# Kernel tuning notes

Hardware: AMD Instinct MI355X
Metric: run time of the kernel (lower is better)

## Reference

```python
import jax, jax.numpy as jnp
import numpy as np

N, D, E, TOP_K = 4096, 1024, 8, 2
NEG_INF = -1e38


def setup_inputs() -> dict:
    key = jax.random.key(0)
    ks = jax.random.split(key, 6)
    s = 1.0 / np.sqrt(D)
    return {
        "x": jax.random.normal(ks[0], (N, D), jnp.float32),
        "noise": jax.random.normal(ks[1], (E,), jnp.float32),
        "Wg": jax.random.normal(ks[2], (D, E), jnp.float32) * s,
        "Wn": jax.random.normal(ks[3], (D, E), jnp.float32) * s,
        "We": jax.random.normal(ks[4], (E, D, D), jnp.float32) * s,
        "be": jax.random.normal(ks[5], (E, D), jnp.float32) * 0.01,
    }


def reference(x, noise, Wg, Wn, We, be):
    # Gating: H = Wg(x) + randn(E) * softplus(Wnoise(x))   (Eq. 4-5)
    g = x @ Wg                                      # [N, E]
    H = g + noise[None, :] * jax.nn.softplus(x @ Wn)  # [N, E]
    # Keep top_k entries of H, set the rest to -Inf (scatter of bottom E-k)
    vals, idx = jax.lax.top_k(H, TOP_K)             # [N, k]
    keep = jnp.full_like(H, NEG_INF)
    keep = keep.at[jnp.arange(H.shape[0])[:, None], idx].set(vals)
    G = jax.nn.softmax(keep, axis=1)                # [N, E]; masked entries -> 0
    # Expert outputs; masked experts have G==0 so dense weighted sum matches
    # the sparse per-example loop: out_n = sum_j G[n,j] * expert_j(x_n)
    Y = jnp.einsum('nd,edh->neh', x, We) + be[None, :, :]  # [N, E, D]
    out = jnp.einsum('ne,neh->nh', G, Y)            # [N, D]
    return out
```

## Files before the change

### kernel.cpp

```cpp
#include <hip/hip_runtime.h>
#include <hip/hip_bf16.h>
#include <stdint.h>

#define NR   4096
#define DIM  1024
#define NE   8
#define BM   128
#define BN   128
#define BK   32

typedef __attribute__((ext_vector_type(8))) short  bf16x8;
typedef __attribute__((ext_vector_type(8))) ushort u16x8;
typedef __attribute__((ext_vector_type(4))) float  f32x4;

__device__ __forceinline__ ushort f2bf(float f) {
    union { __hip_bfloat16 h; ushort u; } cv;
    cv.h = __float2bfloat16(f);
    return cv.u;
}

__device__ __forceinline__ void gload16(const void* g, void* l) {
    __builtin_amdgcn_global_load_lds(
        (const __attribute__((address_space(1))) unsigned int*)g,
        (__attribute__((address_space(3))) unsigned int*)l, 16, 0, 0);
}

__global__ __launch_bounds__(256)
void k1_prep(const float* __restrict__ Wg, const float* __restrict__ Wn,
             float* __restrict__ WT, float* __restrict__ out) {
    const int tid = threadIdx.x;
    if (blockIdx.x < 8) {
        const int k    = blockIdx.x * 128 + (tid >> 1);
        const int half = tid & 1;
        const float* src = half ? Wn : Wg;
        const float4* s4 = (const float4*)(src + (size_t)k * NE);
        float4 a = s4[0], b = s4[1];
        float* d = WT + (size_t)half * 8 * DIM;
        d[(size_t)0 * DIM + k] = a.x; d[(size_t)1 * DIM + k] = a.y;
        d[(size_t)2 * DIM + k] = a.z; d[(size_t)3 * DIM + k] = a.w;
        d[(size_t)4 * DIM + k] = b.x; d[(size_t)5 * DIM + k] = b.y;
        d[(size_t)6 * DIM + k] = b.z; d[(size_t)7 * DIM + k] = b.w;
    } else {
        const int vb = blockIdx.x - 8;
        float4 z = {0.f, 0.f, 0.f, 0.f};
        for (int i = vb * 256 + tid; i < NR * DIM / 4; i += 512 * 256)
            ((float4*)out)[i] = z;
    }
}

__global__ __launch_bounds__(256)
void k2_main(const float* __restrict__ We, ushort* __restrict__ WeT,
             const float* __restrict__ x, const float* __restrict__ noise,
             const float* __restrict__ WT, ushort* __restrict__ xbf,
             uint32_t* __restrict__ eid, float2* __restrict__ wpair) {
    __shared__ float smem[64 * 68];
    const int tid = threadIdx.x;
    if (blockIdx.x < 2048) {
        const int b  = blockIdx.x;
        const int e  = b >> 8, kt = (b >> 4) & 15, ct = b & 15;
        const float* src = We + ((size_t)e * DIM + (size_t)kt * 64) * DIM + ct * 64;
#pragma unroll
        for (int j = 0; j < 4; ++j) {
            int idx = tid + j * 256;
            int r = idx >> 4, c4 = idx & 15;
            *(float4*)&smem[r * 68 + c4 * 4] = *(const float4*)(src + (size_t)r * DIM + c4 * 4);
        }
        __syncthreads();
        ushort* dst = WeT + ((size_t)e * DIM + (size_t)ct * 64) * DIM + kt * 64;
#pragma unroll
        for (int j = 0; j < 2; ++j) {
            int u = tid + j * 256;
            int c = u >> 3, ch = u & 7;
            ushort tmp[8];
#pragma unroll
            for (int q = 0; q < 8; ++q) tmp[q] = f2bf(smem[(ch * 8 + q) * 68 + c]);
            *(u16x8*)(dst + (size_t)c * DIM + ch * 8) = *(u16x8*)tmp;
        }
    } else {
        const int w = tid >> 6, l = tid & 63;
        const int row = (blockIdx.x - 2048) * 4 + w;
        const float* xr = x + (size_t)row * DIM;

        float4 xv[4];
#pragma unroll
        for (int q = 0; q < 4; ++q) xv[q] = *(const float4*)(xr + q * 256 + l * 4);
#pragma unroll
        for (int q = 0; q < 4; ++q) {
            ushort4 xb;
            xb.x = f2bf(xv[q].x); xb.y = f2bf(xv[q].y);
            xb.z = f2bf(xv[q].z); xb.w = f2bf(xv[q].w);
            *(ushort4*)(xbf + (size_t)row * DIM + q * 256 + l * 4) = xb;
        }

        float acc[16];
#pragma unroll
        for (int u = 0; u < 16; ++u) {
            const float* wr_ = WT + (size_t)u * DIM + l * 4;
            float s = 0.f;
#pragma unroll
            for (int q = 0; q < 4; ++q) {
                float4 wv = *(const float4*)(wr_ + q * 256);
                s += xv[q].x * wv.x + xv[q].y * wv.y + xv[q].z * wv.z + xv[q].w * wv.w;
            }
            acc[u] = s;
        }
#pragma unroll
        for (int u = 0; u < 16; ++u) smem[(w * 64 + l) * 17 + u] = acc[u];
        asm volatile("s_waitcnt lgkmcnt(0)" ::: "memory");
        const int c = l >> 4, u = l & 15;
        float v = 0.f;
#pragma unroll
        for (int i = 0; i < 16; ++i) v += smem[(w * 64 + c * 16 + i) * 17 + u];
        v += __shfl_xor(v, 16, 64);
        v += __shfl_xor(v, 32, 64);

        const int e = l & 7;
        float ag = __shfl(v, e, 64);
        float an = __shfl(v, e + 8, 64);
        float sp = (an > 0.f) ? (an + log1pf(expf(-an))) : log1pf(expf(an));
        float H  = ag + noise[e] * sp;

        float Hh[8];
#pragma unroll
        for (int k = 0; k < 8; ++k) Hh[k] = __shfl(H, k, 64);
        if (l == 0) {
            int e0 = 0; float v0 = Hh[0];
#pragma unroll
            for (int k = 1; k < 8; ++k) if (Hh[k] > v0) { v0 = Hh[k]; e0 = k; }
            int e1 = -1; float v1 = 0.f;
#pragma unroll
            for (int k = 0; k < 8; ++k)
                if (k != e0 && (e1 < 0 || Hh[k] > v1)) { v1 = Hh[k]; e1 = k; }
            float rr = expf(v1 - v0);
            float w0 = 1.f / (1.f + rr), w1 = 1.f - w0;
            eid[row] = (uint32_t)e0 | ((uint32_t)e1 << 8);
            float2 wp; wp.x = w0; wp.y = w1;
            wpair[row] = wp;
        }
    }
}

__global__ __launch_bounds__(1024)
void bucket_build(const uint32_t* __restrict__ eid, const float2* __restrict__ wpair,
                  int* __restrict__ cnt, int* __restrict__ idxl, float* __restrict__ wl) {
    const int ex = blockIdx.x;
    __shared__ int base;
    __shared__ int wsum[16];
    if (threadIdx.x == 0) base = 0;
    const int wid = threadIdx.x >> 6, lane = threadIdx.x & 63;
    int* bidx = idxl + (size_t)ex * NR;
    float* bwl = wl + (size_t)ex * NR;

    for (int c0 = 0; c0 < NR; c0 += 1024) {
        const int row = c0 + threadIdx.x;
        const uint32_t em = eid[row];
        const bool m0 = (int)(em & 255u) == ex;
        const bool m1 = (int)((em >> 8) & 255u) == ex;
        const bool m = m0 || m1;
        const unsigned long long bal = __ballot(m);
        if (lane == 0) wsum[wid] = __popcll(bal);
        __syncthreads();
        int wbase = base;
        for (int i = 0; i < wid; ++i) wbase += wsum[i];
        const int pos = wbase + __popcll(bal & ((1ull << lane) - 1ull));
        if (m) {
            bidx[pos] = row;
            float2 wp = wpair[row];
            bwl[pos]  = m0 ? wp.x : wp.y;
        }
        __syncthreads();
        if (threadIdx.x == 0) {
            int s = 0;
#pragma unroll
            for (int i = 0; i < 16; ++i) s += wsum[i];
            base += s;
        }
        __syncthreads();
    }
    if (threadIdx.x == 0) cnt[ex] = base;
}

__global__ __launch_bounds__(256, 2)
void moe_gemm(const ushort* __restrict__ xbf, const ushort* __restrict__ WeT,
              const float* __restrict__ be, const int* __restrict__ cnt,
              const int* __restrict__ idxl, const float* __restrict__ wl,
              float* __restrict__ out) {
    __shared__ ushort lds[4][256][BK];

    const int q8 = gridDim.x >> 3;
    const int W  = (blockIdx.x & 7) * q8 + (blockIdx.x >> 3);
    const int item = W >> 3, cT = W & 7;

    int bucket = -1, tile = 0, accp = 0;
#pragma unroll
    for (int b = 0; b < NE; ++b) {
        int t = (cnt[b] + BM - 1) >> 7;
        if (bucket < 0 && item < accp + t) { bucket = b; tile = item - accp; }
        accp += t;
    }
    if (bucket < 0) return;
    const int count  = cnt[bucket];
    const int nrowsv = min(BM, count - tile * BM);
    const int e  = bucket;
    const int c0 = cT * BN;
    const int*   rows = idxl + (size_t)bucket * NR + tile * BM;
    const float* wrow = wl   + (size_t)bucket * NR + tile * BM;

    const int tid = threadIdx.x, wid = tid >> 6, lane = tid & 63;
    const int l16 = lane & 15, lhi = lane >> 4;
    const int wr = (wid >> 1) * 64, wc = (wid & 1) * 64;

    const int fs   = ((lane >> 2) ^ (lane >> 4)) & 3;
    const int csrc = ((lane & 3) ^ fs) * 8;
    const ushort* aptr[2];
    const ushort* bptr[2];
#pragma unroll
    for (int g = 0; g < 2; ++g) {
        int r = g * 64 + wid * 16 + (lane >> 2);
        aptr[g] = xbf + (size_t)rows[min(r, nrowsv - 1)] * DIM + csrc;
        int c = c0 + g * 64 + wid * 16 + (lane >> 2);
        bptr[g] = WeT + ((size_t)(e * DIM + c)) * DIM + csrc;
    }

    f32x4 acc[4][4];
#pragma unroll
    for (int m = 0; m < 4; ++m)
#pragma unroll
        for (int n = 0; n < 4; ++n) { f32x4 z = {0.f, 0.f, 0.f, 0.f}; acc[m][n] = z; }

#define STAGE_A(T, BUFI) do {                                         \
    const int _k = (T) * BK;                                          \
    _Pragma("unroll")                                                 \
    for (int g = 0; g < 2; ++g)                                       \
        gload16(aptr[g] + _k, &lds[(BUFI)][g * 64 + wid * 16][0]);    \
} while (0)
#define STAGE_B(T, BUFI) do {                                         \
    const int _k = (T) * BK;                                          \
    _Pragma("unroll")                                                 \
    for (int g = 0; g < 2; ++g)                                       \
        gload16(bptr[g] + _k, &lds[(BUFI)][128 + g * 64 + wid * 16][0]); \
} while (0)

    const int fr    = (l16 ^ (l16 >> 2)) & 3;
    const int rslot = (lhi ^ fr) * 8;

    const int NT = DIM / BK;
    STAGE_A(0, 0); STAGE_B(0, 0);
    STAGE_A(1, 1); STAGE_B(1, 1);
    STAGE_A(2, 2); STAGE_B(2, 2);
    asm volatile("s_waitcnt vmcnt(8)" ::: "memory");
    __builtin_amdgcn_s_barrier();

    for (int t = 0; t < NT; ++t) {
        const int c = t & 3;
        const ushort* base = &lds[c][0][0];
        bf16x8 af0 = *(const bf16x8*)(base + (wr + 0 * 16 + l16) * BK + rslot);
        bf16x8 af1 = *(const bf16x8*)(base + (wr + 1 * 16 + l16) * BK + rslot);
        bf16x8 bfr[4];
#pragma unroll
        for (int n = 0; n < 4; ++n)
            bfr[n] = *(const bf16x8*)(base + (128 + wc + n * 16 + l16) * BK + rslot);
        if (t + 3 < NT) STAGE_A(t + 3, (t + 3) & 3);
        __builtin_amdgcn_s_barrier();
        asm volatile("s_waitcnt lgkmcnt(0)" ::: "memory");
        __builtin_amdgcn_s_setprio(1);
#pragma unroll
        for (int n = 0; n < 4; ++n)
            acc[0][n] = __builtin_amdgcn_mfma_f32_16x16x32_bf16(af0, bfr[n], acc[0][n], 0, 0, 0);
#pragma unroll
        for (int n = 0; n < 4; ++n)
            acc[1][n] = __builtin_amdgcn_mfma_f32_16x16x32_bf16(af1, bfr[n], acc[1][n], 0, 0, 0);
        __builtin_amdgcn_s_setprio(0);
        __builtin_amdgcn_s_barrier();
        bf16x8 af2 = *(const bf16x8*)(base + (wr + 2 * 16 + l16) * BK + rslot);
        bf16x8 af3 = *(const bf16x8*)(base + (wr + 3 * 16 + l16) * BK + rslot);
        if (t + 3 < NT) STAGE_B(t + 3, (t + 3) & 3);
        __builtin_amdgcn_s_barrier();
        asm volatile("s_waitcnt lgkmcnt(0)" ::: "memory");
        __builtin_amdgcn_s_setprio(1);
#pragma unroll
        for (int n = 0; n < 4; ++n)
            acc[2][n] = __builtin_amdgcn_mfma_f32_16x16x32_bf16(af2, bfr[n], acc[2][n], 0, 0, 0);
#pragma unroll
        for (int n = 0; n < 4; ++n)
            acc[3][n] = __builtin_amdgcn_mfma_f32_16x16x32_bf16(af3, bfr[n], acc[3][n], 0, 0, 0);
        __builtin_amdgcn_s_setprio(0);
        if (t < NT - 3)       asm volatile("s_waitcnt vmcnt(8)" ::: "memory");
        else if (t == NT - 3) asm volatile("s_waitcnt vmcnt(4)" ::: "memory");
        else                  asm volatile("s_waitcnt vmcnt(0)" ::: "memory");
        __builtin_amdgcn_s_barrier();
    }
#undef STAGE_A
#undef STAGE_B

    float bev[4];
#pragma unroll
    for (int n = 0; n < 4; ++n) bev[n] = be[(size_t)e * DIM + c0 + wc + n * 16 + l16];
#pragma unroll
    for (int m = 0; m < 4; ++m) {
#pragma unroll
        for (int r = 0; r < 4; ++r) {
            int rl = wr + m * 16 + lhi * 4 + r;
            if (rl < nrowsv) {
                int   gr = rows[rl];
                float w  = wrow[rl];
                float* op = out + (size_t)gr * DIM + c0 + wc;
#pragma unroll
                for (int n = 0; n < 4; ++n)
                    atomicAdd(&op[n * 16 + l16], w * (acc[m][n][r] + bev[n]));
            }
        }
    }
}

extern "C" void kernel_launch(void* const* d_in, const int* in_sizes, int n_in,
                              void* d_out, int out_size, void* d_ws, size_t ws_size,
                              hipStream_t stream) {
    const float* x     = (const float*)d_in[0];
    const float* noise = (const float*)d_in[1];
    const float* Wg    = (const float*)d_in[2];
    const float* Wn    = (const float*)d_in[3];
    const float* We    = (const float*)d_in[4];
    const float* be    = (const float*)d_in[5];
    float* out = (float*)d_out;

    char* w = (char*)d_ws;
    size_t off = 256;
    int*      cnt   = (int*)w;
    int*      idxl  = (int*)(w + off);      off += (size_t)2 * NE * NR * 4;
    float*    wl    = (float*)(w + off);    off += (size_t)2 * NE * NR * 4;
    uint32_t* eid   = (uint32_t*)(w + off); off += (size_t)NR * 4;
    float2*   wpair = (float2*)(w + off);   off += (size_t)NR * 8;
    off = (off + 255) & ~(size_t)255;
    float*  WT  = (float*)(w + off);  off += (size_t)16 * DIM * 4;
    ushort* xbf = (ushort*)(w + off); off += (size_t)NR * DIM * 2;
    ushort* WeT = (ushort*)(w + off); off += (size_t)NE * DIM * DIM * 2;

    k1_prep<<<520, 256, 0, stream>>>(Wg, Wn, WT, out);
    k2_main<<<3072, 256, 0, stream>>>(We, WeT, x, noise, WT, xbf, eid, wpair);
    bucket_build<<<NE, 1024, 0, stream>>>(eid, wpair, cnt, idxl, wl);
    moe_gemm<<<72 * 8, 256, 0, stream>>>(xbf, WeT, be, cnt, idxl, wl, out);
}
```

Measured before the change: 95.75 us.

## Enlarge MoE GEMM tiles to 256x256 with 8 waves and triple-buffered LDS

Doubles the block tile in both M and N for the expert GEMM and moves to 512 threads arranged as 2x4 waves, each computing a 128x64 sub-tile. The LDS pipeline drops from four static buffers to three dynamically allocated slots, prefetching two k-steps ahead. The goal is more operand reuse per global load and fewer blocks, which means fewer atomic scatter passes. In exchange the grid shrinks to 160 blocks, fewer than the number of CUs. The 96 KB of dynamic LDS per block and the larger accumulator footprint may also limit occupancy and latency hiding.

```diff
diff --git a/kernel.cpp b/kernel.cpp
--- a/kernel.cpp
+++ b/kernel.cpp
@@ -5,9 +5,11 @@
 #define NR   4096
 #define DIM  1024
 #define NE   8
-#define BM   128
-#define BN   128
+#define BM   256
+#define BN   256
 #define BK   32
+#define NT   (DIM / BK)
+#define SLOT 16384
 
 typedef __attribute__((ext_vector_type(8))) short  bf16x8;
 typedef __attribute__((ext_vector_type(8))) ushort u16x8;
@@ -180,27 +182,27 @@
     if (threadIdx.x == 0) cnt[ex] = base;
 }
 
-__global__ __launch_bounds__(256, 2)
+__global__ __launch_bounds__(512, 2)
 void moe_gemm(const ushort* __restrict__ xbf, const ushort* __restrict__ WeT,
               const float* __restrict__ be, const int* __restrict__ cnt,
               const int* __restrict__ idxl, const float* __restrict__ wl,
               float* __restrict__ out) {
-    __shared__ ushort lds[4][256][BK];
+    extern __shared__ ushort lds[];
 
     const int q8 = gridDim.x >> 3;
     const int W  = (blockIdx.x & 7) * q8 + (blockIdx.x >> 3);
-    const int item = W >> 3, cT = W & 7;
+    const int item = W >> 2, cT = W & 3;
 
     int bucket = -1, tile = 0, accp = 0;
 #pragma unroll
     for (int b = 0; b < NE; ++b) {
-        int t = (cnt[b] + BM - 1) >> 7;
+        int t = (cnt[b] + BM - 1) >> 8;
         if (bucket < 0 && item < accp + t) { bucket = b; tile = item - accp; }
         accp += t;
     }
     if (bucket < 0) return;
     const int count  = cnt[bucket];
-    const int nrowsv = min(BM, count - tile * BM);
+    const int nrows  = min(BM, count - tile * BM);
     const int e  = bucket;
     const int c0 = cT * BN;
     const int*   rows = idxl + (size_t)bucket * NR + tile * BM;
@@ -208,103 +210,99 @@
 
     const int tid = threadIdx.x, wid = tid >> 6, lane = tid & 63;
     const int l16 = lane & 15, lhi = lane >> 4;
-    const int wr = (wid >> 1) * 64, wc = (wid & 1) * 64;
-
-    const int fs   = ((lane >> 2) ^ (lane >> 4)) & 3;
-    const int csrc = ((lane & 3) ^ fs) * 8;
-    const ushort* aptr[2];
-    const ushort* bptr[2];
-#pragma unroll
-    for (int g = 0; g < 2; ++g) {
-        int r = g * 64 + wid * 16 + (lane >> 2);
-        aptr[g] = xbf + (size_t)rows[min(r, nrowsv - 1)] * DIM + csrc;
-        int c = c0 + g * 64 + wid * 16 + (lane >> 2);
-        bptr[g] = WeT + ((size_t)(e * DIM + c)) * DIM + csrc;
-    }
-
-    f32x4 acc[4][4];
-#pragma unroll
-    for (int m = 0; m < 4; ++m)
+    const int widM = wid >> 2, widN = wid & 3;
+    const int arow = widM * 128, bcol = widN * 64;
+
+    const int srow = tid >> 2;
+    const int csrc = (((tid & 3) ^ (((tid >> 2) ^ (tid >> 4)) & 3)) * 8);
+    const ushort* a0 = xbf + (size_t)rows[min(srow,       nrows - 1)] * DIM + csrc;
+    const ushort* a1 = xbf + (size_t)rows[min(128 + srow, nrows - 1)] * DIM + csrc;
+    const ushort* b0 = WeT + ((size_t)(e * DIM + c0 + srow))       * DIM + csrc;
+    const ushort* b1 = WeT + ((size_t)(e * DIM + c0 + 128 + srow)) * DIM + csrc;
+    const int dA0 = wid * 512, dA1 = 4096 + wid * 512;
+    const int dB0 = 8192 + wid * 512, dB1 = 8192 + 4096 + wid * 512;
+
+    const int fr  = (l16 ^ (l16 >> 2)) & 3;
+    const int rch = (lhi ^ fr) * 8;
+
+    f32x4 acc[8][4];
+#pragma unroll
+    for (int m = 0; m < 8; ++m)
 #pragma unroll
         for (int n = 0; n < 4; ++n) { f32x4 z = {0.f, 0.f, 0.f, 0.f}; acc[m][n] = z; }
 
-#define STAGE_A(T, BUFI) do {                                         \
-    const int _k = (T) * BK;                                          \
-    _Pragma("unroll")                                                 \
-    for (int g = 0; g < 2; ++g)                                       \
-        gload16(aptr[g] + _k, &lds[(BUFI)][g * 64 + wid * 16][0]);    \
-} while (0)
-#define STAGE_B(T, BUFI) do {                                         \
-    const int _k = (T) * BK;                                          \
-    _Pragma("unroll")                                                 \
-    for (int g = 0; g < 2; ++g)                                       \
-        gload16(bptr[g] + _k, &lds[(BUFI)][128 + g * 64 + wid * 16][0]); \
-} while (0)
-
-    const int fr    = (l16 ^ (l16 >> 2)) & 3;
-    const int rslot = (lhi ^ fr) * 8;
-
-    const int NT = DIM / BK;
-    STAGE_A(0, 0); STAGE_B(0, 0);
-    STAGE_A(1, 1); STAGE_B(1, 1);
-    STAGE_A(2, 2); STAGE_B(2, 2);
-    asm volatile("s_waitcnt vmcnt(8)" ::: "memory");
+    gload16(a0,      lds + 0 * SLOT + dA0); gload16(a1,      lds + 0 * SLOT + dA1);
+    gload16(b0,      lds + 0 * SLOT + dB0); gload16(b1,      lds + 0 * SLOT + dB1);
+    gload16(a0 + BK, lds + 1 * SLOT + dA0); gload16(a1 + BK, lds + 1 * SLOT + dA1);
+    gload16(b0 + BK, lds + 1 * SLOT + dB0); gload16(b1 + BK, lds + 1 * SLOT + dB1);
+    asm volatile("s_waitcnt vmcnt(4)" ::: "memory");
     __builtin_amdgcn_s_barrier();
 
+    int cur = 0, stg = 2;
     for (int t = 0; t < NT; ++t) {
-        const int c = t & 3;
-        const ushort* base = &lds[c][0][0];
-        bf16x8 af0 = *(const bf16x8*)(base + (wr + 0 * 16 + l16) * BK + rslot);
-        bf16x8 af1 = *(const bf16x8*)(base + (wr + 1 * 16 + l16) * BK + rslot);
-        bf16x8 bfr[4];
+        const ushort* Ab = lds + cur * SLOT;
+        const ushort* Bb = lds + cur * SLOT + 8192;
+        const bool pf = (t + 2 < NT);
+        const int  ko = (t + 2) * BK;
+
+        bf16x8 af[4], bfr[4];
+#pragma unroll
+        for (int m = 0; m < 4; ++m)
+            af[m] = *(const bf16x8*)(Ab + (arow + m * 16 + l16) * BK + rch);
 #pragma unroll
         for (int n = 0; n < 4; ++n)
-            bfr[n] = *(const bf16x8*)(base + (128 + wc + n * 16 + l16) * BK + rslot);
-        if (t + 3 < NT) STAGE_A(t + 3, (t + 3) & 3);
+            bfr[n] = *(const bf16x8*)(Bb + (bcol + n * 16 + l16) * BK + rch);
+        if (pf) {
+            gload16(a0 + ko, lds + stg * SLOT + dA0);
+            gload16(a1 + ko, lds + stg * SLOT + dA1);
+        }
         __builtin_amdgcn_s_barrier();
         asm volatile("s_waitcnt lgkmcnt(0)" ::: "memory");
         __builtin_amdgcn_s_setprio(1);
 #pragma unroll
-        for (int n = 0; n < 4; ++n)
-            acc[0][n] = __builtin_amdgcn_mfma_f32_16x16x32_bf16(af0, bfr[n], acc[0][n], 0, 0, 0);
-#pragma unroll
-        for (int n = 0; n < 4; ++n)
-            acc[1][n] = __builtin_amdgcn_mfma_f32_16x16x32_bf16(af1, bfr[n], acc[1][n], 0, 0, 0);
+        for (int m = 0; m < 4; ++m)
+#pragma unroll
+            for (int n = 0; n < 4; ++n)
+                acc[m][n] = __builtin_amdgcn_mfma_f32_16x16x32_bf16(af[m], bfr[n], acc[m][n], 0, 0, 0);
         __builtin_amdgcn_s_setprio(0);
         __builtin_amdgcn_s_barrier();
-        bf16x8 af2 = *(const bf16x8*)(base + (wr + 2 * 16 + l16) * BK + rslot);
-        bf16x8 af3 = *(const bf16x8*)(base + (wr + 3 * 16 + l16) * BK + rslot);
-        if (t + 3 < NT) STAGE_B(t + 3, (t + 3) & 3);
+
+#pragma unroll
+        for (int m = 0; m < 4; ++m)
+            af[m] = *(const bf16x8*)(Ab + (arow + (m + 4) * 16 + l16) * BK + rch);
+        if (pf) {
+            gload16(b0 + ko, lds + stg * SLOT + dB0);
+            gload16(b1 + ko, lds + stg * SLOT + dB1);
+        }
         __builtin_amdgcn_s_barrier();
         asm volatile("s_waitcnt lgkmcnt(0)" ::: "memory");
         __builtin_amdgcn_s_setprio(1);
 #pragma unroll
-        for (int n = 0; n < 4; ++n)
-            acc[2][n] = __builtin_amdgcn_mfma_f32_16x16x32_bf16(af2, bfr[n], acc[2][n], 0, 0, 0);
-#pragma unroll
-        for (int n = 0; n < 4; ++n)
-            acc[3][n] = __builtin_amdgcn_mfma_f32_16x16x32_bf16(af3, bfr[n], acc[3][n], 0, 0, 0);
+        for (int m = 0; m < 4; ++m)
+#pragma unroll
+            for (int n = 0; n < 4; ++n)
+                acc[m + 4][n] = __builtin_amdgcn_mfma_f32_16x16x32_bf16(af[m], bfr[n], acc[m + 4][n], 0, 0, 0);
         __builtin_amdgcn_s_setprio(0);
-        if (t < NT - 3)       asm volatile("s_waitcnt vmcnt(8)" ::: "memory");
-        else if (t == NT - 3) asm volatile("s_waitcnt vmcnt(4)" ::: "memory");
-        else                  asm volatile("s_waitcnt vmcnt(0)" ::: "memory");
+        if (pf) asm volatile("s_waitcnt vmcnt(4)" ::: "memory");
+        else    asm volatile("s_waitcnt vmcnt(0)" ::: "memory");
         __builtin_amdgcn_s_barrier();
-    }
-#undef STAGE_A
-#undef STAGE_B
+
+        cur = (cur == 2) ? 0 : cur + 1;
+        stg = (stg == 2) ? 0 : stg + 1;
+    }
 
     float bev[4];
 #pragma unroll
-    for (int n = 0; n < 4; ++n) bev[n] = be[(size_t)e * DIM + c0 + wc + n * 16 + l16];
-#pragma unroll
-    for (int m = 0; m < 4; ++m) {
+    for (int n = 0; n < 4; ++n) bev[n] = be[(size_t)e * DIM + c0 + bcol + n * 16 + l16];
+#pragma unroll
+    for (int m = 0; m < 8; ++m) {
 #pragma unroll
         for (int r = 0; r < 4; ++r) {
-            int rl = wr + m * 16 + lhi * 4 + r;
-            if (rl < nrowsv) {
+            int rl = arow + m * 16 + lhi * 4 + r;
+            if (rl < nrows) {
                 int   gr = rows[rl];
                 float w  = wrow[rl];
-                float* op = out + (size_t)gr * DIM + c0 + wc;
+                float* op = out + (size_t)gr * DIM + c0 + bcol;
 #pragma unroll
                 for (int n = 0; n < 4; ++n)
                     atomicAdd(&op[n * 16 + l16], w * (acc[m][n][r] + bev[n]));
@@ -336,8 +334,12 @@
     ushort* xbf = (ushort*)(w + off); off += (size_t)NR * DIM * 2;
     ushort* WeT = (ushort*)(w + off); off += (size_t)NE * DIM * DIM * 2;
 
+    (void)hipFuncSetAttribute((const void*)moe_gemm,
+                              hipFuncAttributeMaxDynamicSharedMemorySize,
+                              3 * SLOT * (int)sizeof(ushort));
+
     k1_prep<<<520, 256, 0, stream>>>(Wg, Wn, WT, out);
     k2_main<<<3072, 256, 0, stream>>>(We, WeT, x, noise, WT, xbf, eid, wpair);
     bucket_build<<<NE, 1024, 0, stream>>>(eid, wpair, cnt, idxl, wl);
-    moe_gemm<<<72 * 8, 256, 0, stream>>>(xbf, WeT, be, cnt, idxl, wl, out);
-}
+    moe_gemm<<<160, 512, 3 * SLOT * sizeof(ushort), stream>>>(xbf, WeT, be, cnt, idxl, wl, out);
+}
```

New measurement: 94.69 us. About the same (-1.1%).
